# Kernel tuning notes

Hardware: AMD Instinct MI355X
Metric: run time of the kernel (lower is better)

## Reference

```python
import jax, jax.numpy as jnp
import numpy as np

K = 3       # kernel_size
STRIDE = 1


def setup_inputs() -> dict:
    key = jax.random.key(0)
    k1, k2, k3 = jax.random.split(key, 3)
    B, C, H, W = 128, 64, 32, 32
    O = 64
    OH = (H - K) // STRIDE + 1  # 30
    OW = (W - K) // STRIDE + 1  # 30
    x = jax.random.normal(k1, (B, C, H, W), dtype=jnp.float32)
    weight = jax.random.normal(k2, (O, C, OH, OW, K, K), dtype=jnp.float32)
    bias = jax.random.normal(k3, (O, OH, OW), dtype=jnp.float32)
    return {"x": x, "weight": weight, "bias": bias}


def reference(x, weight, bias):
    # x: [B, C, H, W]; weight: [O, C, OH, OW, K, K]; bias: [O, OH, OW]
    O, C, OH, OW, _, _ = weight.shape
    # Extract all k x k patches in one pass: [B, C*K*K, OH, OW],
    # feature axis ordered (C, kh, kw) with spatial fastest.
    patches = jax.lax.conv_general_dilated_patches(
        x, filter_shape=(K, K), window_strides=(STRIDE, STRIDE), padding="VALID"
    )
    # Faithful to torch einsum 'bcih,coih->bo': the region's channel axis is
    # contracted against the weight's FIRST axis (nominal out_channels), and the
    # output channel is the weight's SECOND axis (requires C == O).
    # Rearrange weight -> [C*K*K (contract), O (output), OH, OW].
    w = jnp.transpose(weight, (0, 4, 5, 1, 2, 3)).reshape(C * K * K, O, OH, OW)
    out = jnp.einsum("bpij,poij->boij", patches, w) + bias[None]
    return out  # [B, O, OH, OW]
```

## Files before the change

kernel.cpp:

```cpp
#include <hip/hip_runtime.h>


typedef __bf16 bf16x8 __attribute__((ext_vector_type(8)));
typedef float f32x4 __attribute__((ext_vector_type(4)));
typedef unsigned long long u64;
typedef unsigned int u32t;
typedef unsigned short u16t;

struct __attribute__((packed, aligned(8))) uf4 { f32x4 v; };
struct __attribute__((packed, aligned(4))) uf4a { f32x4 v; };
struct __attribute__((packed, aligned(8))) uf2 { float2 v; };
struct __attribute__((packed, aligned(4))) uq2 { u64 x, y; };
struct __attribute__((aligned(16))) ull2 { u64 x, y; };

__device__ __forceinline__ u16t f2bf(float f) {
  union { float f; u32t u; } v; v.f = f;
  u32t r = v.u + 0x7fffu + ((v.u >> 16) & 1u);
  return (u16t)(r >> 16);
}
__device__ __forceinline__ u32t pk2(float a, float b) {
  return (u32t)f2bf(a) | ((u32t)f2bf(b) << 16);
}
__device__ __forceinline__ bf16x8 mk_af(u64 lo, u64 hi) {
  union { u64 q[2]; bf16x8 v; } u;
  u.q[0] = lo; u.q[1] = hi;
  return u.v;
}


__global__ __launch_bounds__(256) void lcl_prep_x(const float* __restrict__ x,
                                                  u16t* __restrict__ Xb) {
  int gid = blockIdx.x * 256 + threadIdx.x;
  int b  = gid & 127;
  int ch = gid >> 7;
  const float* src = x + (size_t)b * 65536 + ch * 32;
  u16t* dst = Xb + (size_t)gid * 32;
  u64 qv[8];
#pragma unroll
  for (int s = 0; s < 8; ++s) {
    f32x4 a = ((const uf4*)(src + s * 4))->v;
    qv[s] = (u64)pk2(a[0], a[1]) | ((u64)pk2(a[2], a[3]) << 32);
  }
#pragma unroll
  for (int s = 0; s < 4; ++s) {
    ull2 w; w.x = qv[2 * s]; w.y = qv[2 * s + 1];
    *(ull2*)(dst + s * 8) = w;
  }
}

__global__ __launch_bounds__(256, 2) void lcl_main(
    const u16t* __restrict__ Xb, const float* __restrict__ wgt,
    const float* __restrict__ bias, float* __restrict__ out) {
  int bid = blockIdx.x;
  int xcd = bid & 7, sg = bid >> 3;
  int t = xcd * 75 + sg;
  int jg = t % 5;
  int r  = t / 5;
  int bg = r & 1, og = (r >> 1) & 1, i = r >> 2;
  int j0 = jg * 6;
  int ij0 = i * 30 + j0;

  __shared__ __align__(16) u16t Bt[2 * 6 * 32 * 104];

  const int tid  = threadIdx.x;
  const int wave = tid >> 6;
  const int lane = tid & 63;
  const int lrow = lane & 15;
  const int q    = lane >> 4;

  {
    u64* zp = (u64*)Bt;
#pragma unroll
    for (int k = 0; k < 39; ++k) zp[tid + k * 256] = 0ull;
  }

  const int b_x = bg * 64 + wave * 16 + lrow;
  const char* xbase = (const char*)Xb;
  u32t xoff[3][2];
#pragma unroll
  for (int s = 0; s < 3; ++s)
#pragma unroll
    for (int tt = 0; tt < 2; ++tt) {
      int g = s * 8 + q * 2 + tt, cc = g / 3, kh = g - cc * 3;
      xoff[s][tt] = (u32t)(((cc * 32 + (i + kh)) * 128 + b_x) * 64 + j0 * 2);
    }

  const int e8 = tid & 7, g8 = tid >> 3;
  const int o_w = og * 32 + g8;
  const int FO0 = e8 * 4;
  const int FO1 = 22 + e8 * 4;
  int Pofs[8];
#pragma unroll
  for (int jm = 0; jm < 8; ++jm) {
    int F = ((jm & 4) ? FO1 : FO0) + (jm & 3);
    Pofs[jm] = (F / 9) * 3328 + ((F % 9) / 3) * 4 + (F % 3);
  }
  const float* wb = wgt + (size_t)o_w * 8100 + ij0 * 9;

  uq2   rq[3][2];
  f32x4 wreg[16];

#define LOAD_CHUNK(C0)                                                      \
  {                                                                         \
    const size_t xadv = (size_t)(C0) * 262144;                              \
    _Pragma("unroll") for (int s = 0; s < 3; ++s)                           \
    _Pragma("unroll") for (int tt = 0; tt < 2; ++tt)                        \
      rq[s][tt] = *(const uq2*)(xbase + xadv + xoff[s][tt]);                \
    _Pragma("unroll") for (int k = 0; k < 16; ++k) {                        \
      const int p_ = k >> 1;                                                \
      const float* wq = wb + (size_t)((C0) + p_) * 518400 +                 \
                        ((k & 1) ? FO1 : FO0);                              \
      wreg[k] = ((const uf4a*)wq)->v;                                       \
    }                                                                       \
  }

  f32x4 acc[6][2];
#pragma unroll
  for (int a = 0; a < 6; ++a)
#pragma unroll
    for (int n = 0; n < 2; ++n) acc[a][n] = f32x4{0.f, 0.f, 0.f, 0.f};

  LOAD_CHUNK(0)
  __syncthreads();

  for (int chunk = 0; chunk < 8; ++chunk) {
    u16t* Bb = Bt + (chunk & 1) * 19968 + g8 * 104;
#pragma unroll
    for (int k = 0; k < 16; ++k) {
      const int p_ = k >> 1, h_ = k & 1;
#pragma unroll
      for (int m = 0; m < 4; ++m)
        (Bb + Pofs[h_ * 4 + m])[p_ * 12] = f2bf(wreg[k][m]);
    }

    u64 rb[3][2][2];
#pragma unroll
    for (int s = 0; s < 3; ++s)
#pragma unroll
      for (int tt = 0; tt < 2; ++tt) {
        rb[s][tt][0] = rq[s][tt].x;
        rb[s][tt][1] = rq[s][tt].y;
      }

    __syncthreads();

    if (chunk < 7) LOAD_CHUNK((chunk + 1) * 8)

#pragma unroll
    for (int s = 0; s < 3; ++s) {
#pragma unroll
      for (int jj = 0; jj < 6; ++jj) {
        bf16x8 bfr0 = *(const bf16x8*)&Bt[(chunk & 1) * 19968 + jj * 3328 +
                                          lrow * 104 + s * 32 + q * 8];
        bf16x8 bfr1 = *(const bf16x8*)&Bt[(chunk & 1) * 19968 + jj * 3328 +
                                          (16 + lrow) * 104 + s * 32 + q * 8];
        u64 lo, hi;
        if (jj == 0) {
          lo = rb[s][0][0];
          hi = rb[s][1][0];
        } else if (jj < 4) {
          lo = (rb[s][0][0] >> (16 * jj)) | (rb[s][0][1] << (64 - 16 * jj));
          hi = (rb[s][1][0] >> (16 * jj)) | (rb[s][1][1] << (64 - 16 * jj));
        } else if (jj == 4) {
          lo = rb[s][0][1];
          hi = rb[s][1][1];
        } else {
          lo = rb[s][0][1] >> 16;
          hi = rb[s][1][1] >> 16;
        }
        bf16x8 af = mk_af(lo, hi);
        acc[jj][0] = __builtin_amdgcn_mfma_f32_16x16x32_bf16(af, bfr0, acc[jj][0], 0, 0, 0);
        acc[jj][1] = __builtin_amdgcn_mfma_f32_16x16x32_bf16(af, bfr1, acc[jj][1], 0, 0, 0);
      }
    }
  }

  const int b0 = bg * 64 + wave * 16 + q * 4;
#pragma unroll
  for (int nt = 0; nt < 2; ++nt) {
    int o = og * 32 + nt * 16 + lrow;
    const float* bp = bias + o * 900 + ij0;
    f32x4 b03 = ((const uf4*)bp)->v;
    float2 b45 = ((const uf2*)(bp + 4))->v;
#pragma unroll
    for (int rr = 0; rr < 4; ++rr) {
      float* op = out + (size_t)(b0 + rr) * 57600 + o * 900 + ij0;
      f32x4 r03;
      r03[0] = acc[0][nt][rr] + b03[0];
      r03[1] = acc[1][nt][rr] + b03[1];
      r03[2] = acc[2][nt][rr] + b03[2];
      r03[3] = acc[3][nt][rr] + b03[3];
      float2 r45;
      r45.x = acc[4][nt][rr] + b45.x;
      r45.y = acc[5][nt][rr] + b45.y;
      ((uf4*)op)->v = r03;
      ((uf2*)(op + 4))->v = r45;
    }
  }
}

__global__ __launch_bounds__(256, 2) void lcl_r4(
    const float* __restrict__ x, const float* __restrict__ wgt,
    const float* __restrict__ bias, float* __restrict__ out) {
  int blk = blockIdx.x;
  int xcd = blk & 7, sg = blk >> 3;
  int t = xcd * 56 + (xcd < 2 ? xcd : 2) + sg;
  int i = t / 15;
  int j0 = (t % 15) * 2;
  int ij0 = i * 30 + j0;

  __shared__ __align__(16) u16t Bt[2 * 2 * 64 * 104];

  const int tid  = threadIdx.x;
  const int wave = tid >> 6;
  const int lane = tid & 63;
  const int lrow = lane & 15;
  const int q    = lane >> 4;

  {
    u64* zp = (u64*)Bt;
#pragma unroll
    for (int k = 0; k < 26; ++k) zp[tid + k * 256] = 0ull;
  }

  int xoffF[3][2];
#pragma unroll
  for (int s = 0; s < 3; ++s)
#pragma unroll
    for (int tt = 0; tt < 2; ++tt) {
      int g = s * 8 + q * 2 + tt, cc = g / 3, kh = g - cc * 3;
      xoffF[s][tt] = cc * 1024 + kh * 32;
    }
  const float* xb0 = x + (wave * 32 + lrow) * 65536 + i * 32 + j0;
  const float* xb1 = xb0 + 16 * 65536;

  const int o_w = tid & 63;
  const float* wb0 = wgt + (size_t)wave * 518400 + o_w * 8100 + ij0 * 9;
  const float* wb1 = wb0 + (size_t)4 * 518400;

  f32x4 av[2][3][2];
  f32x4 wv[2][5];

#define LOAD_CHUNK4(C0)                                                       \
  {                                                                           \
    const float* xc0 = xb0 + (C0) * 1024;                                     \
    const float* xc1 = xb1 + (C0) * 1024;                                     \
    _Pragma("unroll") for (int s = 0; s < 3; ++s)                             \
    _Pragma("unroll") for (int tt = 0; tt < 2; ++tt) {                        \
      av[0][s][tt] = ((const uf4*)(xc0 + xoffF[s][tt]))->v;                   \
      av[1][s][tt] = ((const uf4*)(xc1 + xoffF[s][tt]))->v;                   \
    }                                                                         \
    const float* w0 = wb0 + (size_t)(C0) * 518400;                            \
    const float* w1 = wb1 + (size_t)(C0) * 518400;                            \
    _Pragma("unroll") for (int e = 0; e < 4; ++e) {                           \
      wv[0][e] = ((const uf4*)(w0 + e * 4))->v;                               \
      wv[1][e] = ((const uf4*)(w1 + e * 4))->v;                               \
    }                                                                         \
    wv[0][4] = ((const uf4*)(w0 + 14))->v;                                    \
    wv[1][4] = ((const uf4*)(w1 + 14))->v;                                    \
  }

  f32x4 acc[2][2][4];
#pragma unroll
  for (int a = 0; a < 2; ++a)
#pragma unroll
    for (int b = 0; b < 2; ++b)
#pragma unroll
      for (int c = 0; c < 4; ++c) acc[a][b][c] = f32x4{0.f, 0.f, 0.f, 0.f};

  LOAD_CHUNK4(0)

  for (int chunk = 0; chunk < 8; ++chunk) {
    u16t* B = Bt + (chunk & 1) * 13312;
#pragma unroll
    for (int p = 0; p < 2; ++p) {
      int ccl = wave + 4 * p;
      u16t* Bp = B + o_w * 104 + ccl * 12;
      *(u32t*)&Bp[0] = pk2(wv[p][0][0], wv[p][0][1]);
      Bp[2]  = f2bf(wv[p][0][2]);
      Bp[4]  = f2bf(wv[p][0][3]);
      Bp[5]  = f2bf(wv[p][1][0]);
      Bp[6]  = f2bf(wv[p][1][1]);
      *(u32t*)&Bp[8] = pk2(wv[p][1][2], wv[p][1][3]);
      Bp[10] = f2bf(wv[p][2][0]);
      u16t* Bq = Bp + 6656;
      *(u32t*)&Bq[0] = pk2(wv[p][2][1], wv[p][2][2]);
      Bq[2]  = f2bf(wv[p][2][3]);
      Bq[4]  = f2bf(wv[p][3][0]);
      Bq[5]  = f2bf(wv[p][3][1]);
      Bq[6]  = f2bf(wv[p][3][2]);
      *(u32t*)&Bq[8] = pk2(wv[p][3][3], wv[p][4][2]);
      Bq[10] = f2bf(wv[p][4][3]);
    }

    u64 rb[2][3][2];
#pragma unroll
    for (int mt = 0; mt < 2; ++mt)
#pragma unroll
      for (int s = 0; s < 3; ++s)
#pragma unroll
        for (int tt = 0; tt < 2; ++tt) {
          const f32x4 vv = av[mt][s][tt];
          rb[mt][s][tt] = (u64)pk2(vv[0], vv[1]) | ((u64)pk2(vv[2], vv[3]) << 32);
        }

    __syncthreads();

    if (chunk < 7) LOAD_CHUNK4((chunk + 1) * 8)

#pragma unroll
    for (int s = 0; s < 3; ++s) {
      bf16x8 bfr[2][4];
#pragma unroll
      for (int jj = 0; jj < 2; ++jj)
#pragma unroll
        for (int nt = 0; nt < 4; ++nt)
          bfr[jj][nt] = *reinterpret_cast<const bf16x8*>(
              &B[jj * 6656 + (nt * 16 + lrow) * 104 + s * 32 + q * 8]);
#pragma unroll
      for (int mt = 0; mt < 2; ++mt)
#pragma unroll
        for (int jj = 0; jj < 2; ++jj) {
          u64 lo = rb[mt][s][0] >> (jj * 16);
          u64 hi = rb[mt][s][1] >> (jj * 16);
          bf16x8 af = mk_af(lo, hi);
#pragma unroll
          for (int nt = 0; nt < 4; ++nt)
            acc[mt][jj][nt] = __builtin_amdgcn_mfma_f32_16x16x32_bf16(
                af, bfr[jj][nt], acc[mt][jj][nt], 0, 0, 0);
        }
    }
  }

#pragma unroll
  for (int nt = 0; nt < 4; ++nt) {
    int o = nt * 16 + lrow;
    float2 bv = *(const float2*)(bias + o * 900 + ij0);
#pragma unroll
    for (int mt = 0; mt < 2; ++mt) {
#pragma unroll
      for (int rr = 0; rr < 4; ++rr) {
        int b = wave * 32 + mt * 16 + q * 4 + rr;
        float2 res;
        res.x = acc[mt][0][nt][rr] + bv.x;
        res.y = acc[mt][1][nt][rr] + bv.y;
        *(float2*)(out + b * 57600 + o * 900 + ij0) = res;
      }
    }
  }
}

extern "C" void kernel_launch(void* const* d_in, const int* in_sizes, int n_in,
                              void* d_out, int out_size, void* d_ws,
                              size_t ws_size, hipStream_t stream) {
  const float* x    = (const float*)d_in[0];
  const float* wgt  = (const float*)d_in[1];
  const float* bias = (const float*)d_in[2];
  float* out        = (float*)d_out;
  if (ws_size >= (size_t)16777216 && d_ws != nullptr) {
    lcl_prep_x<<<dim3(1024), dim3(256), 0, stream>>>(x, (u16t*)d_ws);
    lcl_main<<<dim3(600), dim3(256), 0, stream>>>((const u16t*)d_ws, wgt, bias, out);
  } else {
    lcl_r4<<<dim3(450), dim3(256), 0, stream>>>(x, wgt, bias, out);
  }
}
```

Measured before the change: 284.4 us.

## Pre-split bf16 input into overlapping aligned column windows for 16-byte loads

The prep kernel now writes the bf16 input as five overlapping 8-column windows per row, with batch as the inner stride. This lets the main kernel fetch each row slice with one aligned 16-byte load instead of an unaligned packed load. The LDS tile stride is padded (3328 to 3344) to change the bank mapping, and the epilogue writes each batch row as a float4 plus a float2. The cost is a larger workspace (20 MB) and extra write traffic in the prep kernel, and the new path only runs when the workspace is that large.

```diff
diff --git a/kernel.cpp b/kernel.cpp
--- a/kernel.cpp
+++ b/kernel.cpp
@@ -28,27 +28,28 @@
 }
 
 
-__global__ __launch_bounds__(256) void lcl_prep_x(const float* __restrict__ x,
-                                                  u16t* __restrict__ Xb) {
+__global__ __launch_bounds__(256) void lcl_prep_x3(const float* __restrict__ x,
+                                                   u16t* __restrict__ Xb) {
   int gid = blockIdx.x * 256 + threadIdx.x;
   int b  = gid & 127;
   int ch = gid >> 7;
   const float* src = x + (size_t)b * 65536 + ch * 32;
-  u16t* dst = Xb + (size_t)gid * 32;
   u64 qv[8];
 #pragma unroll
   for (int s = 0; s < 8; ++s) {
     f32x4 a = ((const uf4*)(src + s * 4))->v;
     qv[s] = (u64)pk2(a[0], a[1]) | ((u64)pk2(a[2], a[3]) << 32);
   }
-#pragma unroll
-  for (int s = 0; s < 4; ++s) {
-    ull2 w; w.x = qv[2 * s]; w.y = qv[2 * s + 1];
-    *(ull2*)(dst + s * 8) = w;
-  }
-}
-
-__global__ __launch_bounds__(256, 2) void lcl_main(
+  u16t* dst = Xb + ((size_t)ch * 5 * 128 + b) * 8;
+  ull2 w;
+  w.x = qv[0];                          w.y = qv[1];                          *(ull2*)(dst)        = w;
+  w.x = (qv[1] >> 32) | (qv[2] << 32);  w.y = (qv[2] >> 32) | (qv[3] << 32);  *(ull2*)(dst + 1024) = w;
+  w.x = qv[3];                          w.y = qv[4];                          *(ull2*)(dst + 2048) = w;
+  w.x = (qv[4] >> 32) | (qv[5] << 32);  w.y = (qv[5] >> 32) | (qv[6] << 32);  *(ull2*)(dst + 3072) = w;
+  w.x = qv[6];                          w.y = qv[7];                          *(ull2*)(dst + 4096) = w;
+}
+
+__global__ __launch_bounds__(256, 2) void lcl_main10(
     const u16t* __restrict__ Xb, const float* __restrict__ wgt,
     const float* __restrict__ bias, float* __restrict__ out) {
   int bid = blockIdx.x;
@@ -60,7 +61,7 @@
   int j0 = jg * 6;
   int ij0 = i * 30 + j0;
 
-  __shared__ __align__(16) u16t Bt[2 * 6 * 32 * 104];
+  __shared__ __align__(16) u16t Bt[2 * 20480];
 
   const int tid  = threadIdx.x;
   const int wave = tid >> 6;
@@ -71,7 +72,7 @@
   {
     u64* zp = (u64*)Bt;
 #pragma unroll
-    for (int k = 0; k < 39; ++k) zp[tid + k * 256] = 0ull;
+    for (int k = 0; k < 40; ++k) zp[tid + k * 256] = 0ull;
   }
 
   const int b_x = bg * 64 + wave * 16 + lrow;
@@ -82,7 +83,7 @@
 #pragma unroll
     for (int tt = 0; tt < 2; ++tt) {
       int g = s * 8 + q * 2 + tt, cc = g / 3, kh = g - cc * 3;
-      xoff[s][tt] = (u32t)(((cc * 32 + (i + kh)) * 128 + b_x) * 64 + j0 * 2);
+      xoff[s][tt] = (u32t)((((cc * 32 + (i + kh)) * 5 + jg) * 128 + b_x) * 16);
     }
 
   const int e8 = tid & 7, g8 = tid >> 3;
@@ -93,6 +94,177 @@
 #pragma unroll
   for (int jm = 0; jm < 8; ++jm) {
     int F = ((jm & 4) ? FO1 : FO0) + (jm & 3);
+    Pofs[jm] = (F / 9) * 3344 + ((F % 9) / 3) * 4 + (F % 3);
+  }
+  const float* wb = wgt + (size_t)o_w * 8100 + ij0 * 9;
+
+  ull2  rq[3][2];
+  f32x4 wreg[16];
+
+#define LOAD_CHUNK10(C0)                                                    \
+  {                                                                         \
+    const size_t xadv = (size_t)(C0) * 327680;                              \
+    _Pragma("unroll") for (int s = 0; s < 3; ++s)                           \
+    _Pragma("unroll") for (int tt = 0; tt < 2; ++tt)                        \
+      rq[s][tt] = *(const ull2*)(xbase + xadv + xoff[s][tt]);               \
+    _Pragma("unroll") for (int k = 0; k < 16; ++k) {                        \
+      const int p_ = k >> 1;                                                \
+      const float* wq = wb + (size_t)((C0) + p_) * 518400 +                 \
+                        ((k & 1) ? FO1 : FO0);                              \
+      wreg[k] = ((const uf4a*)wq)->v;                                       \
+    }                                                                       \
+  }
+
+  f32x4 acc[6][2];
+#pragma unroll
+  for (int a = 0; a < 6; ++a)
+#pragma unroll
+    for (int n = 0; n < 2; ++n) acc[a][n] = f32x4{0.f, 0.f, 0.f, 0.f};
+
+  LOAD_CHUNK10(0)
+  __syncthreads();
+
+  for (int chunk = 0; chunk < 8; ++chunk) {
+    u16t* Bb = Bt + (chunk & 1) * 20480 + g8 * 104;
+#pragma unroll
+    for (int k = 0; k < 16; ++k) {
+      const int p_ = k >> 1, h_ = k & 1;
+#pragma unroll
+      for (int m = 0; m < 4; ++m)
+        (Bb + Pofs[h_ * 4 + m])[p_ * 12] = f2bf(wreg[k][m]);
+    }
+
+    u64 rb[3][2][2];
+#pragma unroll
+    for (int s = 0; s < 3; ++s)
+#pragma unroll
+      for (int tt = 0; tt < 2; ++tt) {
+        rb[s][tt][0] = rq[s][tt].x;
+        rb[s][tt][1] = rq[s][tt].y;
+      }
+
+    __syncthreads();
+
+    if (chunk < 7) LOAD_CHUNK10((chunk + 1) * 8)
+
+#pragma unroll
+    for (int s = 0; s < 3; ++s) {
+#pragma unroll
+      for (int jj = 0; jj < 6; ++jj) {
+        bf16x8 bfr0 = *(const bf16x8*)&Bt[(chunk & 1) * 20480 + jj * 3344 +
+                                          lrow * 104 + s * 32 + q * 8];
+        bf16x8 bfr1 = *(const bf16x8*)&Bt[(chunk & 1) * 20480 + jj * 3344 +
+                                          (16 + lrow) * 104 + s * 32 + q * 8];
+        u64 lo, hi;
+        if (jj == 0) {
+          lo = rb[s][0][0];
+          hi = rb[s][1][0];
+        } else if (jj < 4) {
+          lo = (rb[s][0][0] >> (16 * jj)) | (rb[s][0][1] << (64 - 16 * jj));
+          hi = (rb[s][1][0] >> (16 * jj)) | (rb[s][1][1] << (64 - 16 * jj));
+        } else if (jj == 4) {
+          lo = rb[s][0][1];
+          hi = rb[s][1][1];
+        } else {
+          lo = rb[s][0][1] >> 16;
+          hi = rb[s][1][1] >> 16;
+        }
+        bf16x8 af = mk_af(lo, hi);
+        acc[jj][0] = __builtin_amdgcn_mfma_f32_16x16x32_bf16(af, bfr0, acc[jj][0], 0, 0, 0);
+        acc[jj][1] = __builtin_amdgcn_mfma_f32_16x16x32_bf16(af, bfr1, acc[jj][1], 0, 0, 0);
+      }
+    }
+  }
+
+  const int b0 = bg * 64 + wave * 16 + q * 4;
+#pragma unroll
+  for (int nt = 0; nt < 2; ++nt) {
+    int o = og * 32 + nt * 16 + lrow;
+    const float* bp = bias + o * 900 + ij0;
+    f32x4 b03 = ((const uf4*)bp)->v;
+    float2 b45 = ((const uf2*)(bp + 4))->v;
+#pragma unroll
+    for (int rr = 0; rr < 4; ++rr) {
+      float* op = out + (size_t)(b0 + rr) * 57600 + o * 900 + ij0;
+      f32x4 r03;
+      r03[0] = acc[0][nt][rr] + b03[0];
+      r03[1] = acc[1][nt][rr] + b03[1];
+      r03[2] = acc[2][nt][rr] + b03[2];
+      r03[3] = acc[3][nt][rr] + b03[3];
+      float2 r45;
+      r45.x = acc[4][nt][rr] + b45.x;
+      r45.y = acc[5][nt][rr] + b45.y;
+      ((uf4*)op)->v = r03;
+      ((uf2*)(op + 4))->v = r45;
+    }
+  }
+}
+
+__global__ __launch_bounds__(256) void lcl_prep_x(const float* __restrict__ x,
+                                                  u16t* __restrict__ Xb) {
+  int gid = blockIdx.x * 256 + threadIdx.x;
+  int b  = gid & 127;
+  int ch = gid >> 7;
+  const float* src = x + (size_t)b * 65536 + ch * 32;
+  u16t* dst = Xb + (size_t)gid * 32;
+  u64 qv[8];
+#pragma unroll
+  for (int s = 0; s < 8; ++s) {
+    f32x4 a = ((const uf4*)(src + s * 4))->v;
+    qv[s] = (u64)pk2(a[0], a[1]) | ((u64)pk2(a[2], a[3]) << 32);
+  }
+#pragma unroll
+  for (int s = 0; s < 4; ++s) {
+    ull2 w; w.x = qv[2 * s]; w.y = qv[2 * s + 1];
+    *(ull2*)(dst + s * 8) = w;
+  }
+}
+
+__global__ __launch_bounds__(256, 2) void lcl_main9(
+    const u16t* __restrict__ Xb, const float* __restrict__ wgt,
+    const float* __restrict__ bias, float* __restrict__ out) {
+  int bid = blockIdx.x;
+  int xcd = bid & 7, sg = bid >> 3;
+  int t = xcd * 75 + sg;
+  int jg = t % 5;
+  int r  = t / 5;
+  int bg = r & 1, og = (r >> 1) & 1, i = r >> 2;
+  int j0 = jg * 6;
+  int ij0 = i * 30 + j0;
+
+  __shared__ __align__(16) u16t Bt[2 * 6 * 32 * 104];
+
+  const int tid  = threadIdx.x;
+  const int wave = tid >> 6;
+  const int lane = tid & 63;
+  const int lrow = lane & 15;
+  const int q    = lane >> 4;
+
+  {
+    u64* zp = (u64*)Bt;
+#pragma unroll
+    for (int k = 0; k < 39; ++k) zp[tid + k * 256] = 0ull;
+  }
+
+  const int b_x = bg * 64 + wave * 16 + lrow;
+  const char* xbase = (const char*)Xb;
+  u32t xoff[3][2];
+#pragma unroll
+  for (int s = 0; s < 3; ++s)
+#pragma unroll
+    for (int tt = 0; tt < 2; ++tt) {
+      int g = s * 8 + q * 2 + tt, cc = g / 3, kh = g - cc * 3;
+      xoff[s][tt] = (u32t)(((cc * 32 + (i + kh)) * 128 + b_x) * 64 + j0 * 2);
+    }
+
+  const int e8 = tid & 7, g8 = tid >> 3;
+  const int o_w = og * 32 + g8;
+  const int FO0 = e8 * 4;
+  const int FO1 = 22 + e8 * 4;
+  int Pofs[8];
+#pragma unroll
+  for (int jm = 0; jm < 8; ++jm) {
+    int F = ((jm & 4) ? FO1 : FO0) + (jm & 3);
     Pofs[jm] = (F / 9) * 3328 + ((F % 9) / 3) * 4 + (F % 3);
   }
   const float* wb = wgt + (size_t)o_w * 8100 + ij0 * 9;
@@ -100,7 +272,7 @@
   uq2   rq[3][2];
   f32x4 wreg[16];
 
-#define LOAD_CHUNK(C0)                                                      \
+#define LOAD_CHUNK9(C0)                                                     \
   {                                                                         \
     const size_t xadv = (size_t)(C0) * 262144;                              \
     _Pragma("unroll") for (int s = 0; s < 3; ++s)                           \
@@ -120,7 +292,7 @@
 #pragma unroll
     for (int n = 0; n < 2; ++n) acc[a][n] = f32x4{0.f, 0.f, 0.f, 0.f};
 
-  LOAD_CHUNK(0)
+  LOAD_CHUNK9(0)
   __syncthreads();
 
   for (int chunk = 0; chunk < 8; ++chunk) {
@@ -144,7 +316,7 @@
 
     __syncthreads();
 
-    if (chunk < 7) LOAD_CHUNK((chunk + 1) * 8)
+    if (chunk < 7) LOAD_CHUNK9((chunk + 1) * 8)
 
 #pragma unroll
     for (int s = 0; s < 3; ++s) {
@@ -357,9 +529,12 @@
   const float* wgt  = (const float*)d_in[1];
   const float* bias = (const float*)d_in[2];
   float* out        = (float*)d_out;
-  if (ws_size >= (size_t)16777216 && d_ws != nullptr) {
+  if (ws_size >= (size_t)20971520 && d_ws != nullptr) {
+    lcl_prep_x3<<<dim3(1024), dim3(256), 0, stream>>>(x, (u16t*)d_ws);
+    lcl_main10<<<dim3(600), dim3(256), 0, stream>>>((const u16t*)d_ws, wgt, bias, out);
+  } else if (ws_size >= (size_t)16777216 && d_ws != nullptr) {
     lcl_prep_x<<<dim3(1024), dim3(256), 0, stream>>>(x, (u16t*)d_ws);
-    lcl_main<<<dim3(600), dim3(256), 0, stream>>>((const u16t*)d_ws, wgt, bias, out);
+    lcl_main9<<<dim3(600), dim3(256), 0, stream>>>((const u16t*)d_ws, wgt, bias, out);
   } else {
     lcl_r4<<<dim3(450), dim3(256), 0, stream>>>(x, wgt, bias, out);
   }
```

After: 276.6 us. 2.7% less time.
